# Optimization experiments

Measured on AMD Instinct MI355X. Metric: run time of the kernel, lower is better.

Reference implementation:

```python
import jax, jax.numpy as jnp
import numpy as np

D_MODEL = 256; D_INNER = 512; D_STATE = 32; D_CONV = 4
NHEADS = 8; HEADDIM = 64; NLAYERS = 2
CONV_DIM = D_INNER + 2 * D_STATE          # 576
ZX = 2 * D_INNER + 2 * D_STATE + NHEADS   # 1096
BSZ = 4; SEQ = 2048
EPS = 1e-5


def _causal_conv(x, w, b):
    # depthwise causal conv: x (b,l,c), w (c,k), b (c,)
    k = w.shape[1]
    L = x.shape[1]
    xp = jnp.pad(x, ((0, 0), (k - 1, 0), (0, 0)))
    out = jnp.zeros_like(x)
    for i in range(k):
        out = out + xp[:, i:i + L, :] * w[:, i]
    return out + b


def _mamba2(u, in_w, conv_w, conv_b, dt_bias, A_log, Dvec, gnorm_w, out_w):
    bsz, l, _ = u.shape
    zxbcdt = jnp.einsum('bld,ed->ble', u, in_w)  # (b,l,ZX)
    z = zxbcdt[..., :D_INNER]
    xBC = zxbcdt[..., D_INNER:D_INNER + CONV_DIM]
    dt = jax.nn.softplus(zxbcdt[..., D_INNER + CONV_DIM:] + dt_bias)  # (b,l,h)
    xBC = jax.nn.silu(_causal_conv(xBC, conv_w, conv_b))
    xs = xBC[..., :D_INNER].reshape(bsz, l, NHEADS, HEADDIM)
    Bm = xBC[..., D_INNER:D_INNER + D_STATE]   # (b,l,n)
    Cm = xBC[..., D_INNER + D_STATE:]          # (b,l,n)
    A = -jnp.exp(A_log)                         # (h,)
    dA = jnp.exp(dt * A)                        # (b,l,h)
    dtx = dt[..., None] * xs                    # (b,l,h,p)

    def step(h, inp):
        dA_t, dtx_t, B_t, C_t = inp
        h = h * dA_t[:, :, None, None] + dtx_t[..., None] * B_t[:, None, None, :]
        y_t = jnp.einsum('bhpn,bn->bhp', h, C_t)
        return h, y_t

    h0 = jnp.zeros((bsz, NHEADS, HEADDIM, D_STATE), u.dtype)
    _, ys = jax.lax.scan(step, h0, (dA.swapaxes(0, 1), dtx.swapaxes(0, 1),
                                    Bm.swapaxes(0, 1), Cm.swapaxes(0, 1)))
    y = ys.swapaxes(0, 1) + Dvec[None, None, :, None] * xs
    y = y.reshape(bsz, l, D_INNER)
    y = y * jax.nn.silu(z)                       # gated RMSNorm (Mamba2 default)
    y = y * jax.lax.rsqrt(jnp.mean(y * y, axis=-1, keepdims=True) + EPS) * gnorm_w
    return jnp.einsum('ble,de->bld', y, out_w)


def _encoder(x, padding_mask, in_w, conv_w, conv_b, dt_bias, A_log, Dvec,
             gnorm_w, out_w, ln_w, ln_b):
    mask = padding_mask[..., None]

    def ln(h):
        mu = jnp.mean(h, -1, keepdims=True)
        var = jnp.mean((h - mu) ** 2, -1, keepdims=True)
        return (h - mu) * jax.lax.rsqrt(var + EPS) * ln_w + ln_b

    for i in range(NLAYERS):
        h = ln(x)
        of = _mamba2(h, in_w[i, 0], conv_w[i, 0], conv_b[i, 0], dt_bias[i, 0],
                     A_log[i, 0], Dvec[i, 0], gnorm_w[i, 0], out_w[i, 0])
        ob = jnp.flip(_mamba2(jnp.flip(h, 1), in_w[i, 1], conv_w[i, 1],
                              conv_b[i, 1], dt_bias[i, 1], A_log[i, 1],
                              Dvec[i, 1], gnorm_w[i, 1], out_w[i, 1]), 1)
        x = x + jnp.where(mask, 0.0, of + ob)
    return jnp.where(mask, 0.0, ln(x))


def setup_inputs() -> dict:
    key = jax.random.key(0)
    ks = jax.random.split(key, 8)
    s = 0.02
    x = jax.random.normal(ks[0], (BSZ, SEQ, D_MODEL), jnp.float32)
    padding_mask = jax.random.randint(ks[1], (BSZ, SEQ), 0, 2) > 0
    in_w = jax.random.normal(ks[2], (NLAYERS, 2, ZX, D_MODEL), jnp.float32) * s
    conv_w = jax.random.normal(ks[3], (NLAYERS, 2, CONV_DIM, D_CONV), jnp.float32) * s
    conv_b = jnp.zeros((NLAYERS, 2, CONV_DIM), jnp.float32)
    dt_bias = jax.random.normal(ks[4], (NLAYERS, 2, NHEADS), jnp.float32) * 0.1
    A_log = jnp.log(jax.random.uniform(ks[5], (NLAYERS, 2, NHEADS), jnp.float32, 1.0, 16.0))
    Dvec = jnp.ones((NLAYERS, 2, NHEADS), jnp.float32)
    gnorm_w = jnp.ones((NLAYERS, 2, D_INNER), jnp.float32)
    out_w = jax.random.normal(ks[6], (NLAYERS, 2, D_MODEL, D_INNER), jnp.float32) * s
    ln_w = jnp.ones((D_MODEL,), jnp.float32)
    ln_b = jnp.zeros((D_MODEL,), jnp.float32)
    return {"x": x, "padding_mask": padding_mask, "in_w": in_w, "conv_w": conv_w,
            "conv_b": conv_b, "dt_bias": dt_bias, "A_log": A_log, "Dvec": Dvec,
            "gnorm_w": gnorm_w, "out_w": out_w, "ln_w": ln_w, "ln_b": ln_b}


def reference(x, padding_mask, in_w, conv_w, conv_b, dt_bias, A_log, Dvec,
              gnorm_w, out_w, ln_w, ln_b):
    return _encoder(x, padding_mask, in_w, conv_w, conv_b, dt_bias, A_log,
                    Dvec, gnorm_w, out_w, ln_w, ln_b)
```

## Files before the change

### kernel.cpp

```cpp
#include <hip/hip_runtime.h>
#include <hip/hip_bf16.h>
#include <math.h>

#define SEQL 2048
#define NB 4
#define DMm 256
#define DIi 512
#define DSs 32
#define NHH 8
#define HDD 64
#define CDD 576
#define ZXD 1096
#define ZXT 2192
#define NPAD 2304
#define NLAY 2
#define QC 64
#define NCH 32
#define RT 8192
#define EPSV 1e-5f

typedef __hip_bfloat16 bf16_t;
using short8 = __attribute__((ext_vector_type(8))) short;
using f32x4  = __attribute__((ext_vector_type(4))) float;

__device__ __forceinline__ float bf16bits2f(short u) {
  union { unsigned int i; float f; } v;
  v.i = ((unsigned int)(unsigned short)u) << 16;
  return v.f;
}

__device__ __forceinline__ int torig(int d, int c, int s) {
  int v = c * QC + s;
  return d ? (SEQL - 1 - v) : v;
}

__device__ __forceinline__ int is_masked(const void* mask, const int* mflag, int r) {
  return (*mflag) ? (int)(((const unsigned char*)mask)[r] != 0)
                  : (int)(((const int*)mask)[r] != 0);
}

__global__ void setup_kernel(const unsigned char* __restrict__ m, int* __restrict__ flag,
                             const float* __restrict__ in_w, const float* __restrict__ out_w,
                             bf16_t* __restrict__ inw_bf, bf16_t* __restrict__ wcat_bf) {
  if (blockIdx.x == 0) {
    __shared__ int any;
    if (threadIdx.x == 0) any = 0;
    __syncthreads();
    int a = 0;
    for (int i = threadIdx.x; i < RT; i += blockDim.x)
      if ((i & 3) && m[i]) a = 1;
    if (a) atomicOr(&any, 1);
    __syncthreads();
    if (threadIdx.x == 0) *flag = any;
  }
  const int n1 = NLAY * NPAD * DMm;
  const int n2 = NLAY * DMm * 1024;
  for (int idx = blockIdx.x * blockDim.x + threadIdx.x; idx < n1 + n2; idx += gridDim.x * blockDim.x) {
    if (idx < n1) {
      int l = idx / (NPAD * DMm);
      int rem = idx % (NPAD * DMm);
      int r = rem / DMm, k = rem % DMm;
      inw_bf[idx] = __float2bfloat16(r < ZXT ? in_w[((size_t)l * ZXT + r) * DMm + k] : 0.f);
    } else {
      int j = idx - n1;
      int l = j / (DMm * 1024);
      int rem = j % (DMm * 1024);
      int dd = rem >> 10, k = rem & 1023;
      int dir = k >> 9, e = k & 511;
      wcat_bf[j] = __float2bfloat16(out_w[((size_t)((l * 2 + dir) * DMm) + dd) * DIi + e]);
    }
  }
}

__global__ __launch_bounds__(256) void ln_kernel(const float* __restrict__ x, bf16_t* __restrict__ h,
                          const float* __restrict__ lnw, const float* __restrict__ lnb) {
  int r = blockIdx.x * 4 + (threadIdx.x >> 6), lane = threadIdx.x & 63;
  float4 v = ((const float4*)(x + (size_t)r * DMm))[lane];
  float s = v.x + v.y + v.z + v.w;
  #pragma unroll
  for (int o = 32; o; o >>= 1) s += __shfl_xor(s, o);
  float mu = s * (1.f / DMm);
  float d0 = v.x - mu, d1 = v.y - mu, d2 = v.z - mu, d3 = v.w - mu;
  float q = d0*d0 + d1*d1 + d2*d2 + d3*d3;
  #pragma unroll
  for (int o = 32; o; o >>= 1) q += __shfl_xor(q, o);
  float rstd = rsqrtf(q * (1.f / DMm) + EPSV);
  float4 w  = ((const float4*)lnw)[lane];
  float4 bb = ((const float4*)lnb)[lane];
  union { bf16_t o4[4]; uint2 u; } out;
  out.o4[0] = __float2bfloat16(d0 * rstd * w.x + bb.x);
  out.o4[1] = __float2bfloat16(d1 * rstd * w.y + bb.y);
  out.o4[2] = __float2bfloat16(d2 * rstd * w.z + bb.z);
  out.o4[3] = __float2bfloat16(d3 * rstd * w.w + bb.w);
  ((uint2*)(h + (size_t)r * DMm))[lane] = out.u;
}

__global__ __launch_bounds__(256) void final_ln(const float* __restrict__ x, const void* __restrict__ mask,
                         const int* __restrict__ mflag,
                         const float* __restrict__ lnw, const float* __restrict__ lnb,
                         float* __restrict__ out) {
  int r = blockIdx.x * 4 + (threadIdx.x >> 6), lane = threadIdx.x & 63;
  float4 v = ((const float4*)(x + (size_t)r * DMm))[lane];
  float s = v.x + v.y + v.z + v.w;
  #pragma unroll
  for (int o = 32; o; o >>= 1) s += __shfl_xor(s, o);
  float mu = s * (1.f / DMm);
  float d0 = v.x - mu, d1 = v.y - mu, d2 = v.z - mu, d3 = v.w - mu;
  float q = d0*d0 + d1*d1 + d2*d2 + d3*d3;
  #pragma unroll
  for (int o = 32; o; o >>= 1) q += __shfl_xor(q, o);
  float rstd = rsqrtf(q * (1.f / DMm) + EPSV);
  float4 w  = ((const float4*)lnw)[lane];
  float4 bb = ((const float4*)lnb)[lane];
  float4 o4;
  if (is_masked(mask, mflag, r)) { o4.x = o4.y = o4.z = o4.w = 0.f; }
  else {
    o4.x = d0 * rstd * w.x + bb.x; o4.y = d1 * rstd * w.y + bb.y;
    o4.z = d2 * rstd * w.z + bb.z; o4.w = d3 * rstd * w.w + bb.w;
  }
  ((float4*)(out + (size_t)r * DMm))[lane] = o4;
}

__global__ __launch_bounds__(256) void gemm_in(const bf16_t* __restrict__ A,
    const bf16_t* __restrict__ Bw, bf16_t* __restrict__ zx, float* __restrict__ dtf) {
  __shared__ __align__(16) bf16_t As[128][72];
  __shared__ __align__(16) bf16_t Bs[128][72];
  int L = blockIdx.y * 18 + blockIdx.x;
  int qx = L & 7, jx = L >> 3;
  int Lp = qx * 144 + jx;
  int n0 = (Lp % 18) * 128, m0 = (Lp / 18) * 128;
  int tid = threadIdx.x, lane = tid & 63, wid = tid >> 6;
  int wm = wid >> 1, wn = wid & 1;
  f32x4 acc[4][4] = {};
  int sr = tid >> 1, sh = (tid & 1) * 32;
  for (int k0 = 0; k0 < DMm; k0 += 64) {
    #pragma unroll
    for (int i = 0; i < 4; i++) {
      *(short8*)&As[sr][sh + i * 8] = *(const short8*)(A + (size_t)(m0 + sr) * DMm + k0 + sh + i * 8);
      *(short8*)&Bs[sr][sh + i * 8] = *(const short8*)(Bw + (size_t)(n0 + sr) * DMm + k0 + sh + i * 8);
    }
    __syncthreads();
    #pragma unroll
    for (int kk = 0; kk < 2; kk++) {
      short8 af[4], bf[4];
      #pragma unroll
      for (int mi = 0; mi < 4; mi++)
        af[mi] = *(const short8*)&As[wm * 64 + mi * 16 + (lane & 15)][kk * 32 + (lane >> 4) * 8];
      #pragma unroll
      for (int ni = 0; ni < 4; ni++)
        bf[ni] = *(const short8*)&Bs[wn * 64 + ni * 16 + (lane & 15)][kk * 32 + (lane >> 4) * 8];
      #pragma unroll
      for (int mi = 0; mi < 4; mi++)
        #pragma unroll
        for (int ni = 0; ni < 4; ni++)
          acc[mi][ni] = __builtin_amdgcn_mfma_f32_16x16x32_bf16(af[mi], bf[ni], acc[mi][ni], 0, 0, 0);
    }
    __syncthreads();
  }
  #pragma unroll
  for (int mi = 0; mi < 4; mi++) {
    #pragma unroll
    for (int ni = 0; ni < 4; ni++) {
      int col = n0 + wn * 64 + ni * 16 + (lane & 15);
      if (col < ZXT) {
        #pragma unroll
        for (int j = 0; j < 4; j++) {
          int row = m0 + wm * 64 + mi * 16 + (lane >> 4) * 4 + j;
          float v = acc[mi][ni][j];
          zx[(size_t)row * ZXT + col] = __float2bfloat16(v);
          if (col >= 1088 && col < 1096)
            dtf[(size_t)row * NHH + (col - 1088)] = v;
          else if (col >= 2184)
            dtf[((size_t)RT + row) * NHH + (col - 2184)] = v;
        }
      }
    }
  }
}

template<int INIT>
__global__ __launch_bounds__(256) void gemm_out(const bf16_t* __restrict__ A, const bf16_t* __restrict__ Bw,
    float* __restrict__ C, const float* __restrict__ init, int ldc,
    const void* __restrict__ mask, const int* __restrict__ mflag) {
  __shared__ __align__(16) bf16_t As[64][72];
  __shared__ __align__(16) bf16_t Bs[64][72];
  const int K = 1024;
  int L = blockIdx.y * 4 + blockIdx.x;
  int Lp = (L & 7) * 64 + (L >> 3);
  int n0 = (Lp & 3) * 64, m0 = (Lp >> 2) * 64;
  int tid = threadIdx.x, lane = tid & 63, wid = tid >> 6;
  f32x4 acc[4] = {};
  int sr = tid >> 2, sk = (tid & 3) * 16;
  for (int k0 = 0; k0 < K; k0 += 64) {
    *(short8*)&As[sr][sk]     = *(const short8*)(A + (size_t)(m0 + sr) * K + k0 + sk);
    *(short8*)&As[sr][sk + 8] = *(const short8*)(A + (size_t)(m0 + sr) * K + k0 + sk + 8);
    *(short8*)&Bs[sr][sk]     = *(const short8*)(Bw + (size_t)(n0 + sr) * K + k0 + sk);
    *(short8*)&Bs[sr][sk + 8] = *(const short8*)(Bw + (size_t)(n0 + sr) * K + k0 + sk + 8);
    __syncthreads();
    #pragma unroll
    for (int kk = 0; kk < 2; kk++) {
      short8 af = *(const short8*)&As[wid * 16 + (lane & 15)][kk * 32 + (lane >> 4) * 8];
      #pragma unroll
      for (int nt = 0; nt < 4; nt++) {
        short8 bf = *(const short8*)&Bs[nt * 16 + (lane & 15)][kk * 32 + (lane >> 4) * 8];
        acc[nt] = __builtin_amdgcn_mfma_f32_16x16x32_bf16(af, bf, acc[nt], 0, 0, 0);
      }
    }
    __syncthreads();
  }
  #pragma unroll
  for (int nt = 0; nt < 4; nt++) {
    int col = n0 + nt * 16 + (lane & 15);
    #pragma unroll
    for (int j = 0; j < 4; j++) {
      int row = m0 + wid * 16 + (lane >> 4) * 4 + j;
      if (INIT) {
        float base = init[(size_t)row * ldc + col];
        C[(size_t)row * ldc + col] = base + (is_masked(mask, mflag, row) ? 0.f : acc[nt][j]);
      } else {
        if (!is_masked(mask, mflag, row)) C[(size_t)row * ldc + col] += acc[nt][j];
      }
    }
  }
}

__global__ __launch_bounds__(256) void chunk_p1(const bf16_t* __restrict__ zx,
    const float* __restrict__ conv_w, const float* __restrict__ conv_b,
    const float* __restrict__ dtf, const float* __restrict__ dt_bias,
    const float* __restrict__ A_log, const float* __restrict__ Dvec,
    bf16_t* __restrict__ ybuf, bf16_t* __restrict__ Sbuf, float* __restrict__ lgbuf,
    float* __restrict__ Pbuf, bf16_t* __restrict__ cbuf, int layer) {
  int c = blockIdx.x, hd = blockIdx.y, b = blockIdx.z;
  int h = hd >> 1, d = hd & 1;
  int tid = threadIdx.x, lane = tid & 63, wid = tid >> 6;
  int rb = b * SEQL;
  __shared__ __align__(16) bf16_t Bs[QC][40];
  __shared__ __align__(16) bf16_t Cs[QC][40];
  __shared__ __align__(16) bf16_t Xt[QC][72];
  __shared__ __align__(16) char shraw[19968];
  bf16_t (*rawX)[64]  = (bf16_t(*)[64])shraw;
  bf16_t (*rawBC)[64] = (bf16_t(*)[64])(shraw + 8576);
  float (*cw4)[4]     = (float(*)[4])(shraw + 17152);
  float *cbv          = (float*)(shraw + 19200);
  bf16_t (*Ms)[72]    = (bf16_t(*)[72])shraw;
  bf16_t (*Btw)[72]   = (bf16_t(*)[72])(shraw + 9216);
  __shared__ float lam[QC], dts[QC], wss[QC];

  for (int i = tid; i < 67 * 8; i += 256) {
    int s = i >> 3, p0 = (i & 7) * 8;
    int v = c * QC + s - 3;
    short8 xv = {0,0,0,0,0,0,0,0}, bcv = {0,0,0,0,0,0,0,0};
    if (v >= 0) {
      int t = d ? (SEQL - 1 - v) : v;
      const bf16_t* rowp = zx + (size_t)(rb + t) * ZXT + d * ZXD + DIi;
      xv  = *(const short8*)(rowp + h * HDD + p0);
      bcv = *(const short8*)(rowp + 512 + p0);
    }
    *(short8*)&rawX[s][p0]  = xv;
    *(short8*)&rawBC[s][p0] = bcv;
  }
  if (tid < 128) {
    int cch = (tid < 64) ? (h * HDD + tid) : (512 + (tid - 64));
    const float* wp = conv_w + ((size_t)((layer * 2 + d) * CDD) + cch) * 4;
    *(float4*)cw4[tid] = *(const float4*)wp;
    cbv[tid] = conv_b[(layer * 2 + d) * CDD + cch];
  }
  if (tid < QC) {
    int ro = rb + torig(d, c, tid);
    size_t rr = (size_t)d * RT + ro;
    float xv = dtf[rr * NHH + h] + dt_bias[(layer * 2 + d) * NHH + h];
    float dtv = (xv > 20.f) ? xv : log1pf(expf(xv));
    float Ah = -expf(A_log[(layer * 2 + d) * NHH + h]);
    float la = dtv * Ah;
    dts[tid] = dtv;
    #pragma unroll
    for (int o = 1; o < 64; o <<= 1) { float vv = __shfl_up(la, o); if (tid >= o) la += vv; }
    lam[tid] = la;
    Pbuf[rr * NHH + h] = expf(la);
    float lq = __shfl(la, 63);
    wss[tid] = expf(lq - la) * dtv;
    if (tid == 63) lgbuf[((b * NHH + h) * 2 + d) * NCH + c] = la;
  }
  __syncthreads();

  {
    int p = tid & 63, sg = tid >> 6;
    #pragma unroll
    for (int half = 0; half < 2; half++) {
      int s0 = sg * 16 + half * 8;
      union { bf16_t h8[8]; short8 v; } ox;
      #pragma unroll
      for (int j = 0; j < 8; j++) {
        int s = s0 + j;
        float a = cbv[p];
        #pragma unroll
        for (int ii = 0; ii < 4; ii++)
          a += __bfloat162float(rawX[s + ii][p]) * cw4[p][ii];
        a = a / (1.f + expf(-a));
        ox.h8[j] = __float2bfloat16(a);
      }
      *(short8*)&Xt[p][s0] = ox.v;
    }
  }
  for (int i = tid; i < QC * HDD; i += 256) {
    int s = i >> 6, q = i & 63;
    float a = cbv[64 + q];
    #pragma unroll
    for (int ii = 0; ii < 4; ii++)
      a += __bfloat162float(rawBC[s + ii][q]) * cw4[64 + q][ii];
    a = a / (1.f + expf(-a));
    bf16_t av = __float2bfloat16(a);
    if (q < DSs) Bs[s][q] = av; else Cs[s][q - DSs] = av;
  }
  __syncthreads();

  {
    short8 cf = *(const short8*)&Cs[wid * 16 + (lane & 15)][(lane >> 4) * 8];
    int sbase = lane & 15;
    #pragma unroll
    for (int sc = 0; sc < 4; sc++) {
      int s = sc * 16 + sbase;
      if (sc <= wid) {
        short8 bfr = *(const short8*)&Bs[s][(lane >> 4) * 8];
        f32x4 g = {};
        g = __builtin_amdgcn_mfma_f32_16x16x32_bf16(cf, bfr, g, 0, 0, 0);
        float ls = lam[s], dv = dts[s];
        #pragma unroll
        for (int j = 0; j < 4; j++) {
          int t = wid * 16 + (lane >> 4) * 4 + j;
          float m = (s <= t) ? expf(lam[t] - ls) * dv * g[j] : 0.f;
          Ms[t][s] = __float2bfloat16(m);
        }
      } else {
        #pragma unroll
        for (int j = 0; j < 4; j++) Ms[wid * 16 + (lane >> 4) * 4 + j][s] = __float2bfloat16(0.f);
      }
    }
  }
  for (int i = tid; i < DSs * QC; i += 256) {
    int n = i >> 6, s = i & 63;
    Btw[n][s] = __float2bfloat16(wss[s] * __bfloat162float(Bs[s][n]));
  }
  if (h == 0) {
    for (int i = tid; i < QC * DSs; i += 256) {
      int s = i >> 5, n = i & 31;
      cbuf[((size_t)(d * RT + rb + torig(d, c, s))) * DSs + n] = Cs[s][n];
    }
  }
  __syncthreads();

  float Dv = Dvec[(layer * 2 + d) * NHH + h];
  {
    short8 ma0 = *(const short8*)&Ms[wid * 16 + (lane & 15)][(lane >> 4) * 8];
    short8 ma1 = *(const short8*)&Ms[wid * 16 + (lane & 15)][32 + (lane >> 4) * 8];
    int t0 = wid * 16 + (lane >> 4) * 4;
    #pragma unroll
    for (int pt = 0; pt < 4; pt++) {
      short8 xb0 = *(const short8*)&Xt[pt * 16 + (lane & 15)][(lane >> 4) * 8];
      short8 xb1 = *(const short8*)&Xt[pt * 16 + (lane & 15)][32 + (lane >> 4) * 8];
      f32x4 ya = {};
      ya = __builtin_amdgcn_mfma_f32_16x16x32_bf16(ma0, xb0, ya, 0, 0, 0);
      ya = __builtin_amdgcn_mfma_f32_16x16x32_bf16(ma1, xb1, ya, 0, 0, 0);
      int p = pt * 16 + (lane & 15);
      union { uint2 u; short s4[4]; } xr;
      xr.u = *(const uint2*)&Xt[p][t0];
      #pragma unroll
      for (int j = 0; j < 4; j++) {
        int t = t0 + j;
        float xv = bf16bits2f(xr.s4[j]);
        ybuf[((size_t)(d * RT + rb + torig(d, c, t))) * DIi + h * HDD + p] =
            __float2bfloat16(ya[j] + Dv * xv);
      }
    }
  }
  {
    short8 xa0 = *(const short8*)&Xt[wid * 16 + (lane & 15)][(lane >> 4) * 8];
    short8 xa1 = *(const short8*)&Xt[wid * 16 + (lane & 15)][32 + (lane >> 4) * 8];
    size_t base = ((size_t)((b * NHH + h) * 2 + d) * NCH + c) * 2048;
    #pragma unroll
    for (int nt = 0; nt < 2; nt++) {
      short8 bw0 = *(const short8*)&Btw[nt * 16 + (lane & 15)][(lane >> 4) * 8];
      short8 bw1 = *(const short8*)&Btw[nt * 16 + (lane & 15)][32 + (lane >> 4) * 8];
      f32x4 sa = {};
      sa = __builtin_amdgcn_mfma_f32_16x16x32_bf16(xa0, bw0, sa, 0, 0, 0);
      sa = __builtin_amdgcn_mfma_f32_16x16x32_bf16(xa1, bw1, sa, 0, 0, 0);
      int n = nt * 16 + (lane & 15);
      #pragma unroll
      for (int j = 0; j < 4; j++) {
        int p = wid * 16 + (lane >> 4) * 4 + j;
        Sbuf[base + (size_t)p * DSs + n] = __float2bfloat16(sa[j]);
      }
    }
  }
}

__global__ __launch_bounds__(256) void chunk_p2b(const bf16_t* __restrict__ Sbuf,
    const float* __restrict__ lgbuf, bf16_t* __restrict__ Hbuf) {
  int bhd = blockIdx.x, cb = blockIdx.y;
  int tid = threadIdx.x;
  __shared__ float W[NCH][NCH + 1];
  __shared__ float cum[NCH];
  if (tid < NCH) {
    float la = lgbuf[bhd * NCH + tid];
    #pragma unroll
    for (int o = 1; o < NCH; o <<= 1) { float v = __shfl_up(la, o); if (tid >= o) la += v; }
    cum[tid] = la;
  }
  __syncthreads();
  for (int i = tid; i < NCH * NCH; i += 256) {
    int c = i >> 5, cp = i & 31;
    W[c][cp] = (cp < c) ? expf(cum[c - 1] - cum[cp]) : 0.f;
  }
  __syncthreads();
  int j = cb * 256 + tid;
  const bf16_t* Sb = Sbuf + (size_t)bhd * NCH * 2048;
  bf16_t* Hb = Hbuf + (size_t)bhd * NCH * 2048;
  float H[NCH];
  #pragma unroll
  for (int c = 0; c < NCH; c++) H[c] = 0.f;
  for (int cp = 0; cp < NCH; cp++) {
    float s = __bfloat162float(Sb[(size_t)cp * 2048 + j]);
    #pragma unroll
    for (int c = 0; c < NCH; c++) H[c] += W[c][cp] * s;
  }
  #pragma unroll
  for (int c = 0; c < NCH; c++) Hb[(size_t)c * 2048 + j] = __float2bfloat16(H[c]);
}

__global__ __launch_bounds__(512) void chunk_p3g(const bf16_t* __restrict__ cbuf,
    const bf16_t* __restrict__ ybuf, const float* __restrict__ Pbuf,
    const bf16_t* __restrict__ Hbuf, const bf16_t* __restrict__ zx,
    const float* __restrict__ gnorm, bf16_t* __restrict__ ycat, int layer) {
  int cc = blockIdx.x, d = blockIdx.y, b = blockIdx.z;
  int c = cc >> 1, trow0 = (cc & 1) * 32;
  int tid = threadIdx.x, lane = tid & 63, wid = tid >> 6;
  int rb = b * SEQL;
  __shared__ __align__(16) bf16_t Cs[32][40];
  __shared__ __align__(16) bf16_t Hs[NHH][HDD][40];
  __shared__ __align__(16) bf16_t Ys[32][520];
  __shared__ float Ps[NHH][32];

  for (int i = tid; i < 32 * DSs; i += 512) {
    int s = i >> 5, n = i & 31;
    Cs[s][n] = cbuf[((size_t)(d * RT + rb + torig(d, c, trow0 + s))) * DSs + n];
  }
  for (int i = tid; i < NHH * HDD * DSs; i += 512) {
    int hh = i >> 11, rem = i & 2047;
    Hs[hh][rem >> 5][rem & 31] =
        Hbuf[((size_t)((b * NHH + hh) * 2 + d) * NCH + c) * 2048 + rem];
  }
  if (tid < NHH * 32) {
    int hh = tid >> 5, t = tid & 31;
    Ps[hh][t] = Pbuf[((size_t)(d * RT + rb + torig(d, c, trow0 + t))) * NHH + hh];
  }
  __syncthreads();

  {
    int h = wid;
    #pragma unroll
    for (int tt = 0; tt < 2; tt++) {
      short8 ca = *(const short8*)&Cs[tt * 16 + (lane & 15)][(lane >> 4) * 8];
      #pragma unroll
      for (int pp = 0; pp < 4; pp++) {
        short8 hf = *(const short8*)&Hs[h][pp * 16 + (lane & 15)][(lane >> 4) * 8];
        f32x4 a = {};
        a = __builtin_amdgcn_mfma_f32_16x16x32_bf16(ca, hf, a, 0, 0, 0);
        int p = pp * 16 + (lane & 15);
        #pragma unroll
        for (int j = 0; j < 4; j++) {
          int trel = tt * 16 + (lane >> 4) * 4 + j;
          size_t rr = (size_t)(d * RT + rb + torig(d, c, trow0 + trel));
          float iv = __bfloat162float(ybuf[rr * DIi + h * HDD + p]);
          Ys[trel][h * HDD + p] = __float2bfloat16(iv + Ps[h][trel] * a[j]);
        }
      }
    }
  }
  __syncthreads();

  const float* gw = gnorm + (layer * 2 + d) * DIi;
  #pragma unroll
  for (int rloc = 0; rloc < 4; rloc++) {
    int trel = wid * 4 + rloc;
    int r = rb + torig(d, c, trow0 + trel);
    short8 yv8 = *(const short8*)&Ys[trel][lane * 8];
    short8 zv8 = *(const short8*)(zx + (size_t)r * ZXT + d * ZXD + lane * 8);
    float g[8]; float ss = 0.f;
    #pragma unroll
    for (int j = 0; j < 8; j++) {
      float y = bf16bits2f(yv8[j]);
      float z = bf16bits2f(zv8[j]);
      float v = y * z / (1.f + expf(-z));
      g[j] = v; ss += v * v;
    }
    #pragma unroll
    for (int o = 32; o; o >>= 1) ss += __shfl_xor(ss, o);
    float sc = rsqrtf(ss * (1.f / DIi) + EPSV);
    union { bf16_t o8[8]; uint4 u; } ov;
    #pragma unroll
    for (int j = 0; j < 8; j++)
      ov.o8[j] = __float2bfloat16(g[j] * sc * gw[lane * 8 + j]);
    *(uint4*)(ycat + (size_t)r * 1024 + d * DIi + lane * 8) = ov.u;
  }
}

extern "C" void kernel_launch(void* const* d_in, const int* in_sizes, int n_in,
                              void* d_out, int out_size, void* d_ws, size_t ws_size,
                              hipStream_t stream) {
  const float* x_in    = (const float*)d_in[0];
  const void*  maskp   = (const void*)d_in[1];
  const float* in_w    = (const float*)d_in[2];
  const float* conv_w  = (const float*)d_in[3];
  const float* conv_b  = (const float*)d_in[4];
  const float* dt_bias = (const float*)d_in[5];
  const float* A_log   = (const float*)d_in[6];
  const float* Dvec    = (const float*)d_in[7];
  const float* gnorm_w = (const float*)d_in[8];
  const float* out_w   = (const float*)d_in[9];
  const float* ln_w    = (const float*)d_in[10];
  const float* ln_b    = (const float*)d_in[11];

  char* ws = (char*)d_ws;
  size_t off = 0;
  auto alloc = [&](size_t bytes) -> void* {
    void* p = ws + off; off += (bytes + 255) & ~(size_t)255; return p;
  };
  float*  x_cur   = (float*)alloc((size_t)RT * DMm * 4);
  bf16_t* h_bf    = (bf16_t*)alloc((size_t)RT * DMm * 2);
  bf16_t* zx      = (bf16_t*)alloc((size_t)RT * ZXT * 2);
  bf16_t* cbuf    = (bf16_t*)alloc((size_t)2 * RT * DSs * 2);
  float*  dtf     = (float*)alloc((size_t)2 * RT * NHH * 4);
  float*  Pbuf    = (float*)alloc((size_t)2 * RT * NHH * 4);
  bf16_t* ybuf    = (bf16_t*)alloc((size_t)2 * RT * DIi * 2);
  bf16_t* ycat    = (bf16_t*)alloc((size_t)RT * 1024 * 2);
  bf16_t* Sbuf    = (bf16_t*)alloc((size_t)64 * NCH * 2048 * 2);
  bf16_t* Hbuf    = (bf16_t*)alloc((size_t)64 * NCH * 2048 * 2);
  float*  lgbuf   = (float*)alloc((size_t)64 * NCH * 4);
  bf16_t* inw_bf  = (bf16_t*)alloc((size_t)NLAY * NPAD * DMm * 2);
  bf16_t* wcat_bf = (bf16_t*)alloc((size_t)NLAY * DMm * 1024 * 2);
  int*    mflag   = (int*)alloc(256);

  setup_kernel<<<256, 256, 0, stream>>>((const unsigned char*)maskp, mflag,
                                        in_w, out_w, inw_bf, wcat_bf);

  for (int layer = 0; layer < NLAY; layer++) {
    const float* xsrc = (layer == 0) ? x_in : x_cur;
    ln_kernel<<<RT / 4, 256, 0, stream>>>(xsrc, h_bf, ln_w, ln_b);
    gemm_in<<<dim3(NPAD / 128, RT / 128), 256, 0, stream>>>(
        h_bf, inw_bf + (size_t)layer * NPAD * DMm, zx, dtf);
    chunk_p1<<<dim3(NCH, 16, NB), 256, 0, stream>>>(zx, conv_w, conv_b, dtf, dt_bias,
                                                    A_log, Dvec, ybuf, Sbuf, lgbuf,
                                                    Pbuf, cbuf, layer);
    chunk_p2b<<<dim3(64, 8), 256, 0, stream>>>(Sbuf, lgbuf, Hbuf);
    chunk_p3g<<<dim3(64, 2, NB), 512, 0, stream>>>(cbuf, ybuf, Pbuf, Hbuf, zx,
                                                   gnorm_w, ycat, layer);
    if (layer == 0)
      gemm_out<1><<<dim3(DMm / 64, RT / 64), 256, 0, stream>>>(
          ycat, wcat_bf + (size_t)layer * DMm * 1024, x_cur, x_in,
          DMm, maskp, mflag);
    else
      gemm_out<0><<<dim3(DMm / 64, RT / 64), 256, 0, stream>>>(
          ycat, wcat_bf + (size_t)layer * DMm * 1024, x_cur, nullptr,
          DMm, maskp, mflag);
  }
  final_ln<<<RT / 4, 256, 0, stream>>>(x_cur, maskp, mflag, ln_w, ln_b, (float*)d_out);
}
```

Before: 252.0 us.

## Fuse layer-norm into gemm_out via last-block election; use fast exp intrinsics

Drops the separate per-layer LN kernel and the final LN kernel. Each gemm_out block bumps a per-row-tile atomic counter, and the fourth block to finish a 64-row tile normalizes those rows, writing either the bf16 input for the next layer or the masked final output. It also swaps expf for __expf across the chunk kernels. The cost is threadfence and atomic overhead plus a serialized tail in the elected blocks, and __expf brings a small precision loss.

```diff
diff --git a/kernel.cpp b/kernel.cpp
--- a/kernel.cpp
+++ b/kernel.cpp
@@ -40,9 +40,11 @@
 }
 
 __global__ void setup_kernel(const unsigned char* __restrict__ m, int* __restrict__ flag,
+                             int* __restrict__ cnt,
                              const float* __restrict__ in_w, const float* __restrict__ out_w,
                              bf16_t* __restrict__ inw_bf, bf16_t* __restrict__ wcat_bf) {
   if (blockIdx.x == 0) {
+    cnt[threadIdx.x] = 0;
     __shared__ int any;
     if (threadIdx.x == 0) any = 0;
     __syncthreads();
@@ -95,32 +97,6 @@
   ((uint2*)(h + (size_t)r * DMm))[lane] = out.u;
 }
 
-__global__ __launch_bounds__(256) void final_ln(const float* __restrict__ x, const void* __restrict__ mask,
-                         const int* __restrict__ mflag,
-                         const float* __restrict__ lnw, const float* __restrict__ lnb,
-                         float* __restrict__ out) {
-  int r = blockIdx.x * 4 + (threadIdx.x >> 6), lane = threadIdx.x & 63;
-  float4 v = ((const float4*)(x + (size_t)r * DMm))[lane];
-  float s = v.x + v.y + v.z + v.w;
-  #pragma unroll
-  for (int o = 32; o; o >>= 1) s += __shfl_xor(s, o);
-  float mu = s * (1.f / DMm);
-  float d0 = v.x - mu, d1 = v.y - mu, d2 = v.z - mu, d3 = v.w - mu;
-  float q = d0*d0 + d1*d1 + d2*d2 + d3*d3;
-  #pragma unroll
-  for (int o = 32; o; o >>= 1) q += __shfl_xor(q, o);
-  float rstd = rsqrtf(q * (1.f / DMm) + EPSV);
-  float4 w  = ((const float4*)lnw)[lane];
-  float4 bb = ((const float4*)lnb)[lane];
-  float4 o4;
-  if (is_masked(mask, mflag, r)) { o4.x = o4.y = o4.z = o4.w = 0.f; }
-  else {
-    o4.x = d0 * rstd * w.x + bb.x; o4.y = d1 * rstd * w.y + bb.y;
-    o4.z = d2 * rstd * w.z + bb.z; o4.w = d3 * rstd * w.w + bb.w;
-  }
-  ((float4*)(out + (size_t)r * DMm))[lane] = o4;
-}
-
 __global__ __launch_bounds__(256) void gemm_in(const bf16_t* __restrict__ A,
     const bf16_t* __restrict__ Bw, bf16_t* __restrict__ zx, float* __restrict__ dtf) {
   __shared__ __align__(16) bf16_t As[128][72];
@@ -178,9 +154,11 @@
   }
 }
 
-template<int INIT>
+template<int INIT, int FUSE>
 __global__ __launch_bounds__(256) void gemm_out(const bf16_t* __restrict__ A, const bf16_t* __restrict__ Bw,
-    float* __restrict__ C, const float* __restrict__ init, int ldc,
+    float* __restrict__ C, const float* __restrict__ init, int* __restrict__ cnt,
+    bf16_t* __restrict__ hout, float* __restrict__ fout,
+    const float* __restrict__ lnw, const float* __restrict__ lnb,
     const void* __restrict__ mask, const int* __restrict__ mflag) {
   __shared__ __align__(16) bf16_t As[64][72];
   __shared__ __align__(16) bf16_t Bs[64][72];
@@ -215,10 +193,48 @@
     for (int j = 0; j < 4; j++) {
       int row = m0 + wid * 16 + (lane >> 4) * 4 + j;
       if (INIT) {
-        float base = init[(size_t)row * ldc + col];
-        C[(size_t)row * ldc + col] = base + (is_masked(mask, mflag, row) ? 0.f : acc[nt][j]);
+        float base = init[(size_t)row * DMm + col];
+        C[(size_t)row * DMm + col] = base + (is_masked(mask, mflag, row) ? 0.f : acc[nt][j]);
       } else {
-        if (!is_masked(mask, mflag, row)) C[(size_t)row * ldc + col] += acc[nt][j];
+        if (!is_masked(mask, mflag, row)) C[(size_t)row * DMm + col] += acc[nt][j];
+      }
+    }
+  }
+  __threadfence();
+  __shared__ int elect;
+  if (tid == 0) elect = (atomicAdd(&cnt[m0 >> 6], 1) == 3);
+  __syncthreads();
+  if (elect) {
+    __threadfence();
+    float4 w  = ((const float4*)lnw)[lane];
+    float4 bb = ((const float4*)lnb)[lane];
+    for (int it = 0; it < 16; it++) {
+      int row = m0 + it * 4 + wid;
+      float4 v = ((const float4*)(C + (size_t)row * DMm))[lane];
+      float s = v.x + v.y + v.z + v.w;
+      #pragma unroll
+      for (int o = 32; o; o >>= 1) s += __shfl_xor(s, o);
+      float mu = s * (1.f / DMm);
+      float d0 = v.x - mu, d1 = v.y - mu, d2 = v.z - mu, d3 = v.w - mu;
+      float q = d0*d0 + d1*d1 + d2*d2 + d3*d3;
+      #pragma unroll
+      for (int o = 32; o; o >>= 1) q += __shfl_xor(q, o);
+      float rstd = rsqrtf(q * (1.f / DMm) + EPSV);
+      if (FUSE == 1) {
+        union { bf16_t o4[4]; uint2 u; } ov;
+        ov.o4[0] = __float2bfloat16(d0 * rstd * w.x + bb.x);
+        ov.o4[1] = __float2bfloat16(d1 * rstd * w.y + bb.y);
+        ov.o4[2] = __float2bfloat16(d2 * rstd * w.z + bb.z);
+        ov.o4[3] = __float2bfloat16(d3 * rstd * w.w + bb.w);
+        ((uint2*)(hout + (size_t)row * DMm))[lane] = ov.u;
+      } else {
+        float4 o4;
+        if (is_masked(mask, mflag, row)) { o4.x = o4.y = o4.z = o4.w = 0.f; }
+        else {
+          o4.x = d0 * rstd * w.x + bb.x; o4.y = d1 * rstd * w.y + bb.y;
+          o4.z = d2 * rstd * w.z + bb.z; o4.w = d3 * rstd * w.w + bb.w;
+        }
+        ((float4*)(fout + (size_t)row * DMm))[lane] = o4;
       }
     }
   }
@@ -276,9 +292,9 @@
     #pragma unroll
     for (int o = 1; o < 64; o <<= 1) { float vv = __shfl_up(la, o); if (tid >= o) la += vv; }
     lam[tid] = la;
-    Pbuf[rr * NHH + h] = expf(la);
+    Pbuf[rr * NHH + h] = __expf(la);
     float lq = __shfl(la, 63);
-    wss[tid] = expf(lq - la) * dtv;
+    wss[tid] = __expf(lq - la) * dtv;
     if (tid == 63) lgbuf[((b * NHH + h) * 2 + d) * NCH + c] = la;
   }
   __syncthreads();
@@ -296,7 +312,7 @@
         #pragma unroll
         for (int ii = 0; ii < 4; ii++)
           a += __bfloat162float(rawX[s + ii][p]) * cw4[p][ii];
-        a = a / (1.f + expf(-a));
+        a = a / (1.f + __expf(-a));
         ox.h8[j] = __float2bfloat16(a);
       }
       *(short8*)&Xt[p][s0] = ox.v;
@@ -308,7 +324,7 @@
     #pragma unroll
     for (int ii = 0; ii < 4; ii++)
       a += __bfloat162float(rawBC[s + ii][q]) * cw4[64 + q][ii];
-    a = a / (1.f + expf(-a));
+    a = a / (1.f + __expf(-a));
     bf16_t av = __float2bfloat16(a);
     if (q < DSs) Bs[s][q] = av; else Cs[s][q - DSs] = av;
   }
@@ -328,7 +344,7 @@
         #pragma unroll
         for (int j = 0; j < 4; j++) {
           int t = wid * 16 + (lane >> 4) * 4 + j;
-          float m = (s <= t) ? expf(lam[t] - ls) * dv * g[j] : 0.f;
+          float m = (s <= t) ? __expf(lam[t] - ls) * dv * g[j] : 0.f;
           Ms[t][s] = __float2bfloat16(m);
         }
       } else {
@@ -409,7 +425,7 @@
   __syncthreads();
   for (int i = tid; i < NCH * NCH; i += 256) {
     int c = i >> 5, cp = i & 31;
-    W[c][cp] = (cp < c) ? expf(cum[c - 1] - cum[cp]) : 0.f;
+    W[c][cp] = (cp < c) ? __expf(cum[c - 1] - cum[cp]) : 0.f;
   }
   __syncthreads();
   int j = cb * 256 + tid;
@@ -490,7 +506,7 @@
     for (int j = 0; j < 8; j++) {
       float y = bf16bits2f(yv8[j]);
       float z = bf16bits2f(zv8[j]);
-      float v = y * z / (1.f + expf(-z));
+      float v = y * z / (1.f + __expf(-z));
       g[j] = v; ss += v * v;
     }
     #pragma unroll
@@ -539,13 +555,14 @@
   bf16_t* inw_bf  = (bf16_t*)alloc((size_t)NLAY * NPAD * DMm * 2);
   bf16_t* wcat_bf = (bf16_t*)alloc((size_t)NLAY * DMm * 1024 * 2);
   int*    mflag   = (int*)alloc(256);
-
-  setup_kernel<<<256, 256, 0, stream>>>((const unsigned char*)maskp, mflag,
+  int*    cnt     = (int*)alloc(256 * 4);
+
+  setup_kernel<<<256, 256, 0, stream>>>((const unsigned char*)maskp, mflag, cnt,
                                         in_w, out_w, inw_bf, wcat_bf);
 
   for (int layer = 0; layer < NLAY; layer++) {
-    const float* xsrc = (layer == 0) ? x_in : x_cur;
-    ln_kernel<<<RT / 4, 256, 0, stream>>>(xsrc, h_bf, ln_w, ln_b);
+    if (layer == 0)
+      ln_kernel<<<RT / 4, 256, 0, stream>>>(x_in, h_bf, ln_w, ln_b);
     gemm_in<<<dim3(NPAD / 128, RT / 128), 256, 0, stream>>>(
         h_bf, inw_bf + (size_t)layer * NPAD * DMm, zx, dtf);
     chunk_p1<<<dim3(NCH, 16, NB), 256, 0, stream>>>(zx, conv_w, conv_b, dtf, dt_bias,
@@ -555,13 +572,12 @@
     chunk_p3g<<<dim3(64, 2, NB), 512, 0, stream>>>(cbuf, ybuf, Pbuf, Hbuf, zx,
                                                    gnorm_w, ycat, layer);
     if (layer == 0)
-      gemm_out<1><<<dim3(DMm / 64, RT / 64), 256, 0, stream>>>(
-          ycat, wcat_bf + (size_t)layer * DMm * 1024, x_cur, x_in,
-          DMm, maskp, mflag);
+      gemm_out<1, 1><<<dim3(DMm / 64, RT / 64), 256, 0, stream>>>(
+          ycat, wcat_bf + (size_t)layer * DMm * 1024, x_cur, x_in, cnt,
+          h_bf, nullptr, ln_w, ln_b, maskp, mflag);
     else
-      gemm_out<0><<<dim3(DMm / 64, RT / 64), 256, 0, stream>>>(
-          ycat, wcat_bf + (size_t)layer * DMm * 1024, x_cur, nullptr,
-          DMm, maskp, mflag);
-  }
-  final_ln<<<RT / 4, 256, 0, stream>>>(x_cur, maskp, mflag, ln_w, ln_b, (float*)d_out);
-}
+      gemm_out<0, 2><<<dim3(DMm / 64, RT / 64), 256, 0, stream>>>(
+          ycat, wcat_bf + (size_t)layer * DMm * 1024, x_cur, nullptr, cnt + 128,
+          nullptr, (float*)d_out, ln_w, ln_b, maskp, mflag);
+  }
+}
```

After: 354.6 us. 1.41x slower.
